# Kernel tuning notes

Hardware: AMD Instinct MI355X
Metric: run time of the kernel (lower is better)

Reference implementation:

```python
import jax, jax.numpy as jnp
import numpy as np

B, S, E, H = 4, 2048, 1024, 16
D = E // H  # head dim = 64


def setup_inputs() -> dict:
    key = jax.random.key(0)
    ks = jax.random.split(key, 5)
    scale = 0.02
    return {
        "x": jax.random.normal(ks[0], (B, S, E), dtype=jnp.float32),
        "Wa_w": jax.random.normal(ks[1], (3 * E, E), dtype=jnp.float32) * scale,
        "Wa_b": jax.random.normal(ks[2], (3 * E,), dtype=jnp.float32) * scale,
        "Wo_w": jax.random.normal(ks[3], (E, E), dtype=jnp.float32) * scale,
        "Wo_b": jax.random.normal(ks[4], (E,), dtype=jnp.float32) * scale,
    }


def reference(x, Wa_w, Wa_b, Wo_w, Wo_b):
    b, s, e = x.shape
    # Fused QKV projection (torch Linear: x @ W^T + b)
    qkv = jnp.einsum("bse,fe->bsf", x, Wa_w) + Wa_b  # [B,S,3E]
    q, k, v = jnp.split(qkv, 3, axis=-1)
    # [B,S,E] -> [B,H,S,D]
    def heads(t):
        return t.reshape(b, s, H, D).transpose(0, 2, 1, 3)
    q, k, v = heads(q), heads(k), heads(v)
    # Causal attention with explicit score matrix (as in the original)
    scores = jnp.einsum("bhqd,bhkd->bhqk", q, k) / jnp.sqrt(jnp.float32(D))
    causal = jnp.tril(jnp.ones((s, s), dtype=bool))
    scores = jnp.where(causal, scores, -jnp.inf)
    attn = jax.nn.softmax(scores, axis=-1)  # dropout p=0 -> identity
    out = jnp.einsum("bhqk,bhkd->bhqd", attn, v)  # [B,H,S,D]
    out = out.transpose(0, 2, 1, 3).reshape(b, s, e)
    return jnp.einsum("bse,fe->bsf", out, Wo_w) + Wo_b
```

## Files before the change

kernel.cpp:

```cpp
#include <hip/hip_runtime.h>
#include <hip/hip_bf16.h>
#include <cstdint>

typedef __bf16 bf16_t;
typedef __attribute__((ext_vector_type(8))) __bf16 bf16x8;
typedef __attribute__((ext_vector_type(4))) __bf16 bf16x4;
typedef __attribute__((ext_vector_type(4))) float f32x4;

#define B_ 4
#define S_ 2048
#define E_ 1024
#define H_ 16
#define D_ 64

#define QSCALE 0.18033688011112042f

__global__ void cvt_all(const float* __restrict__ x, const float* __restrict__ wa,
                        const float* __restrict__ wo,
                        bf16_t* __restrict__ xb, bf16_t* __restrict__ wab,
                        bf16_t* __restrict__ wob) {
    constexpr int N1 = (B_ * S_ * E_) / 4;
    constexpr int N2 = (3 * E_ * E_) / 4;
    constexpr int N3 = (E_ * E_) / 4;
    int i = blockIdx.x * blockDim.x + threadIdx.x;
    int stride = gridDim.x * blockDim.x;
    for (; i < N1 + N2 + N3; i += stride) {
        const float* src; bf16_t* dst; int k;
        if (i < N1) { src = x; dst = xb; k = i; }
        else if (i < N1 + N2) { src = wa; dst = wab; k = i - N1; }
        else { src = wo; dst = wob; k = i - N1 - N2; }
        f32x4 v = reinterpret_cast<const f32x4*>(src)[k];
        bf16x4 o;
        o.x = (bf16_t)v.x; o.y = (bf16_t)v.y; o.z = (bf16_t)v.z; o.w = (bf16_t)v.w;
        reinterpret_cast<bf16x4*>(dst)[k] = o;
    }
}

__device__ __forceinline__ void gload_lds16(const bf16_t* g, bf16_t* l) {
    __builtin_amdgcn_global_load_lds((const __attribute__((address_space(1))) void*)g,
                                     (__attribute__((address_space(3))) void*)l, 16, 0, 0);
}

__device__ __forceinline__ void wait_vm4() { asm volatile("s_waitcnt vmcnt(4)" ::: "memory"); }
__device__ __forceinline__ void wait_vm0() { asm volatile("s_waitcnt vmcnt(0)" ::: "memory"); }

template <int MODE>
__launch_bounds__(256, 3)
__global__ void gemm_pipe(const bf16_t* __restrict__ A, const bf16_t* __restrict__ Bm,
                          const float* __restrict__ bias,
                          int M, int N, int NG,
                          bf16_t* __restrict__ Qg, bf16_t* __restrict__ Kg,
                          bf16_t* __restrict__ Vtg, float* __restrict__ Outf) {
    constexpr int K = 1024, BK = 32, NKT = K / BK;
    constexpr int BM = 128, BN = 128;
    __shared__ __align__(16) bf16_t As[3][BM * BK];
    __shared__ __align__(16) bf16_t Bs[3][BN * BK];

    const int xcd = blockIdx.x & 7;
    const int u = blockIdx.x >> 3;
    const int grp = 8 * NG;
    const int g = u / grp, r2 = u % grp;
    const int ntl = r2 / 8, mtl = r2 & 7;
    const int mt = xcd * 8 + mtl;
    const int nt = g * NG + ntl;
    const int m0 = mt * BM, n0 = nt * BN;

    const int t = threadIdx.x;
    const int lane = t & 63;
    const int wid = t >> 6;
    const int wr = wid >> 1, wc = wid & 1;
    const int lr = lane & 15, lg = lane >> 4;

    auto mkSrc = [&](const bf16_t* base, int c, int row0) {
        const int line = c >> 3, chg = (c & 7) ^ (line & 7);
        return base + (int64_t)(row0 + 2 * line + (chg >> 2)) * K + (chg & 3) * 8;
    };
    const bf16_t* aSrc0 = mkSrc(A, t, m0);
    const bf16_t* aSrc1 = mkSrc(A, t + 256, m0);
    const bf16_t* bSrc0 = mkSrc(Bm, t, n0);
    const bf16_t* bSrc1 = mkSrc(Bm, t + 256, n0);

    auto stageT = [&](int kt, int buf) {
        gload_lds16(aSrc0 + kt * BK, &As[buf][t * 8]);
        gload_lds16(aSrc1 + kt * BK, &As[buf][(t + 256) * 8]);
        gload_lds16(bSrc0 + kt * BK, &Bs[buf][t * 8]);
        gload_lds16(bSrc1 + kt * BK, &Bs[buf][(t + 256) * 8]);
    };

    auto fragOff = [](int row, int kc) -> int {
        const int line = row >> 1;
        const int ch = ((row & 1) << 2) | kc;
        return line * 64 + ((ch ^ (line & 7)) << 3);
    };

    f32x4 acc[4][4] = {};

    stageT(0, 0);
    stageT(1, 1);

    int bufc = 0, bufs = 2;
    for (int kt = 0; kt < NKT; ++kt) {
        if (kt < NKT - 1) wait_vm4(); else wait_vm0();
        __builtin_amdgcn_s_barrier();
        __builtin_amdgcn_sched_barrier(0);

        if (kt + 2 < NKT) stageT(kt + 2, bufs);

        bf16x8 bfr[4], afr[4];
#pragma unroll
        for (int j = 0; j < 4; ++j)
            bfr[j] = *(const bf16x8*)&Bs[bufc][fragOff(wc * 64 + j * 16 + lr, lg)];
#pragma unroll
        for (int i = 0; i < 4; ++i)
            afr[i] = *(const bf16x8*)&As[bufc][fragOff(wr * 64 + i * 16 + lr, lg)];

#pragma unroll
        for (int i = 0; i < 4; ++i)
#pragma unroll
            for (int j = 0; j < 4; ++j)
                acc[i][j] = __builtin_amdgcn_mfma_f32_16x16x32_bf16(afr[i], bfr[j], acc[i][j], 0, 0, 0);

        bufc = (bufc == 2) ? 0 : bufc + 1;
        bufs = (bufs == 2) ? 0 : bufs + 1;
    }

    float bv[4];
#pragma unroll
    for (int j = 0; j < 4; ++j) bv[j] = bias[n0 + wc * 64 + j * 16 + lr];

    if (MODE == 0) {
        const int which = n0 >> 10;
        const int h = (((n0 & 1023) + wc * 64) >> 6);
#pragma unroll
        for (int i = 0; i < 4; ++i) {
#pragma unroll
            for (int r = 0; r < 4; ++r) {
                const int m = m0 + wr * 64 + i * 16 + lg * 4 + r;
                const int b = m >> 11, si = m & (S_ - 1);
                if (which == 0) {
                    bf16_t* p = &Qg[(((int64_t)(b * H_ + h)) * S_ + si) * D_ + lr];
#pragma unroll
                    for (int j = 0; j < 4; ++j)
                        p[j * 16] = (bf16_t)((acc[i][j][r] + bv[j]) * QSCALE);
                } else if (which == 1) {
                    bf16_t* p = &Kg[(((int64_t)(b * H_ + h)) * S_ + si) * D_ + lr];
#pragma unroll
                    for (int j = 0; j < 4; ++j)
                        p[j * 16] = (bf16_t)(acc[i][j][r] + bv[j]);
                } else {
                    bf16_t* p = &Vtg[(((int64_t)(b * H_ + h)) * D_ + lr) * S_ + si];
#pragma unroll
                    for (int j = 0; j < 4; ++j)
                        p[(int64_t)(j * 16) * S_] = (bf16_t)(acc[i][j][r] + bv[j]);
                }
            }
        }
    } else {
#pragma unroll
        for (int i = 0; i < 4; ++i) {
#pragma unroll
            for (int r = 0; r < 4; ++r) {
                const int m = m0 + wr * 64 + i * 16 + lg * 4 + r;
                float* p = &Outf[(int64_t)m * N + n0 + wc * 64 + lr];
#pragma unroll
                for (int j = 0; j < 4; ++j)
                    p[j * 16] = acc[i][j][r] + bv[j];
            }
        }
    }
}

__launch_bounds__(256, 4)
__global__ void attn_causal(const bf16_t* __restrict__ Qg, const bf16_t* __restrict__ Kg,
                            const bf16_t* __restrict__ Vtg, bf16_t* __restrict__ Og) {
    __shared__ __align__(16) bf16_t Ks[2][64 * 64];
    __shared__ __align__(16) bf16_t Vs[2][64 * 64];
    __shared__ __align__(16) bf16_t P_lds[4][16 * 64];

    const int bid = blockIdx.x;
    const int xcd = bid & 7, j = bid >> 3;
    const int bh = (j >> 4) * 8 + xcd;
    const int i = j & 15;
    const int qtA = i, qtB = 31 - i;

    const int t = threadIdx.x, lane = t & 63, w = t >> 6;
    const int lr = lane & 15, lg = lane >> 4;
    const int q0A = qtA * 64 + w * 16;
    const int q0B = qtB * 64 + w * 16;

    const bf16_t* Qb = Qg + (int64_t)bh * S_ * D_;
    const bf16_t* Kb = Kg + (int64_t)bh * S_ * D_;
    const bf16_t* Vb = Vtg + (int64_t)bh * D_ * S_;

    const int srow = t >> 3;
    const int scol_sw = (t & 7) ^ (srow & 7);

    auto stageK = [&](int buf, int kv0) {
        const bf16_t* base = Kb + (kv0 + srow) * D_ + scol_sw * 8;
        gload_lds16(base, &Ks[buf][t * 8]);
        gload_lds16(base + 32 * D_, &Ks[buf][t * 8 + 2048]);
    };
    auto stageV = [&](int buf, int kv0) {
        const bf16_t* base = Vb + srow * S_ + kv0 + scol_sw * 8;
        gload_lds16(base, &Vs[buf][t * 8]);
        gload_lds16(base + 32 * S_, &Vs[buf][t * 8 + 2048]);
    };

    auto psw = [](int row, int col) {
        return row * 64 + ((((col >> 3) ^ (row & 7)) << 3) | (col & 7));
    };

    bf16x8 qfA[2], qfB[2];
#pragma unroll
    for (int kk = 0; kk < 2; ++kk) {
        qfA[kk] = *(const bf16x8*)&Qb[(q0A + lr) * D_ + kk * 32 + lg * 8];
        qfB[kk] = *(const bf16x8*)&Qb[(q0B + lr) * D_ + kk * 32 + lg * 8];
    }

    bf16x8 ones;
#pragma unroll
    for (int e = 0; e < 8; ++e) ones[e] = (bf16_t)1.0f;

    f32x4 oA[4] = {}, oB[4] = {};
    f32x4 lA = {}, lB = {};

    int cur = 0;
    stageK(0, 0);
    stageV(0, 0);
    __syncthreads();

    for (int tkv = 0; tkv <= qtB; ++tkv) {
        const int kv0 = tkv * 64;
        if (tkv < qtB) { stageK(cur ^ 1, kv0 + 64); stageV(cur ^ 1, kv0 + 64); }

        auto process = [&](int q0, const bf16x8* qf, f32x4* o, f32x4& accl, bf16_t* Pw) {
            f32x4 sc[4] = {};
            __builtin_amdgcn_s_setprio(1);
#pragma unroll
            for (int nj = 0; nj < 4; ++nj) {
                if (kv0 + nj * 16 <= q0 + 15) {
                    const int krow = nj * 16 + lr;
#pragma unroll
                    for (int kk = 0; kk < 2; ++kk) {
                        bf16x8 kfr = *(const bf16x8*)&Ks[cur][krow * 64 + (((kk * 4 + lg) ^ (krow & 7)) * 8)];
                        sc[nj] = __builtin_amdgcn_mfma_f32_16x16x32_bf16(qf[kk], kfr, sc[nj], 0, 0, 0);
                    }
                }
            }
            __builtin_amdgcn_s_setprio(0);

            if (kv0 + 64 > q0) {
#pragma unroll
                for (int nj = 0; nj < 4; ++nj) {
                    const int col = kv0 + nj * 16 + lr;
#pragma unroll
                    for (int r = 0; r < 4; ++r) {
                        const int rowg = q0 + lg * 4 + r;
                        if (col > rowg) sc[nj][r] = -1e30f;
                    }
                }
            }

#pragma unroll
            for (int nj = 0; nj < 4; ++nj)
#pragma unroll
                for (int r = 0; r < 4; ++r)
                    Pw[psw(lg * 4 + r, nj * 16 + lr)] = (bf16_t)__builtin_amdgcn_exp2f(sc[nj][r]);
            asm volatile("s_waitcnt lgkmcnt(0)" ::: "memory");
            __builtin_amdgcn_sched_barrier(0);

            __builtin_amdgcn_s_setprio(1);
#pragma unroll
            for (int kk = 0; kk < 2; ++kk) {
                bf16x8 pa = *(const bf16x8*)&Pw[psw(lr, kk * 32 + lg * 8)];
                accl = __builtin_amdgcn_mfma_f32_16x16x32_bf16(pa, ones, accl, 0, 0, 0);
#pragma unroll
                for (int nd = 0; nd < 4; ++nd) {
                    const int vrow = nd * 16 + lr;
                    bf16x8 vf = *(const bf16x8*)&Vs[cur][vrow * 64 + (((kk * 4 + lg) ^ (vrow & 7)) * 8)];
                    o[nd] = __builtin_amdgcn_mfma_f32_16x16x32_bf16(pa, vf, o[nd], 0, 0, 0);
                }
            }
            __builtin_amdgcn_s_setprio(0);
        };

        process(q0B, qfB, oB, lB, &P_lds[w][0]);
        if (tkv <= qtA) process(q0A, qfA, oA, lA, &P_lds[w][0]);

        __syncthreads();
        cur ^= 1;
    }

    const int b = bh >> 4, h = bh & 15;
#pragma unroll
    for (int r = 0; r < 4; ++r) {
        const float rlA = 1.0f / lA[r];
        const float rlB = 1.0f / lB[r];
        const int rA = q0A + lg * 4 + r;
        const int rB = q0B + lg * 4 + r;
#pragma unroll
        for (int nd = 0; nd < 4; ++nd) {
            Og[((int64_t)(b * S_ + rA)) * E_ + h * D_ + nd * 16 + lr] = (bf16_t)(oA[nd][r] * rlA);
            Og[((int64_t)(b * S_ + rB)) * E_ + h * D_ + nd * 16 + lr] = (bf16_t)(oB[nd][r] * rlB);
        }
    }
}

extern "C" void kernel_launch(void* const* d_in, const int* in_sizes, int n_in,
                              void* d_out, int out_size, void* d_ws, size_t ws_size,
                              hipStream_t stream) {
    const float* x    = (const float*)d_in[0];
    const float* Wa_w = (const float*)d_in[1];
    const float* Wa_b = (const float*)d_in[2];
    const float* Wo_w = (const float*)d_in[3];
    const float* Wo_b = (const float*)d_in[4];
    float* out = (float*)d_out;

    const size_t M = (size_t)B_ * S_;
    char* ws = (char*)d_ws;
    bf16_t* xb  = (bf16_t*)ws; ws += M * E_ * 2;
    bf16_t* wab = (bf16_t*)ws; ws += (size_t)3 * E_ * E_ * 2;
    bf16_t* wob = (bf16_t*)ws; ws += (size_t)E_ * E_ * 2;
    bf16_t* Qg  = (bf16_t*)ws; ws += M * E_ * 2;
    bf16_t* Kg  = (bf16_t*)ws; ws += M * E_ * 2;
    bf16_t* Vtg = (bf16_t*)ws; ws += M * E_ * 2;
    bf16_t* Og  = (bf16_t*)ws; ws += M * E_ * 2;

    cvt_all<<<2048, 256, 0, stream>>>(x, Wa_w, Wo_w, xb, wab, wob);

    gemm_pipe<0><<<1536, 256, 0, stream>>>(
        xb, wab, Wa_b, 8192, 3072, 12, Qg, Kg, Vtg, nullptr);

    attn_causal<<<B_ * H_ * 16, 256, 0, stream>>>(Qg, Kg, Vtg, Og);

    gemm_pipe<1><<<512, 256, 0, stream>>>(
        Og, wob, Wo_b, 8192, 1024, 8, nullptr, nullptr, nullptr, out);
}
```

Baseline: 180.2 us.

## Process two M-tiles per GEMM block with continuous cross-tile prefetch

```diff
diff --git a/kernel.cpp b/kernel.cpp
--- a/kernel.cpp
+++ b/kernel.cpp
@@ -51,19 +51,19 @@
                           int M, int N, int NG,
                           bf16_t* __restrict__ Qg, bf16_t* __restrict__ Kg,
                           bf16_t* __restrict__ Vtg, float* __restrict__ Outf) {
-    constexpr int K = 1024, BK = 32, NKT = K / BK;
+    constexpr int K = 1024, BK = 32;
     constexpr int BM = 128, BN = 128;
     __shared__ __align__(16) bf16_t As[3][BM * BK];
     __shared__ __align__(16) bf16_t Bs[3][BN * BK];
 
     const int xcd = blockIdx.x & 7;
     const int u = blockIdx.x >> 3;
-    const int grp = 8 * NG;
+    const int grp = 4 * NG;
     const int g = u / grp, r2 = u % grp;
-    const int ntl = r2 / 8, mtl = r2 & 7;
-    const int mt = xcd * 8 + mtl;
+    const int ntl = r2 >> 2, q = r2 & 3;
+    const int mt0 = xcd * 8 + q;
     const int nt = g * NG + ntl;
-    const int m0 = mt * BM, n0 = nt * BN;
+    const int m0a = mt0 * BM, m0b = (mt0 + 4) * BM, n0 = nt * BN;
 
     const int t = threadIdx.x;
     const int lane = t & 63;
@@ -75,14 +75,19 @@
         const int line = c >> 3, chg = (c & 7) ^ (line & 7);
         return base + (int64_t)(row0 + 2 * line + (chg >> 2)) * K + (chg & 3) * 8;
     };
-    const bf16_t* aSrc0 = mkSrc(A, t, m0);
-    const bf16_t* aSrc1 = mkSrc(A, t + 256, m0);
+    const bf16_t* aSrcA0 = mkSrc(A, t, m0a);
+    const bf16_t* aSrcA1 = mkSrc(A, t + 256, m0a);
+    const bf16_t* aSrcB0 = mkSrc(A, t, m0b);
+    const bf16_t* aSrcB1 = mkSrc(A, t + 256, m0b);
     const bf16_t* bSrc0 = mkSrc(Bm, t, n0);
     const bf16_t* bSrc1 = mkSrc(Bm, t + 256, n0);
 
-    auto stageT = [&](int kt, int buf) {
-        gload_lds16(aSrc0 + kt * BK, &As[buf][t * 8]);
-        gload_lds16(aSrc1 + kt * BK, &As[buf][(t + 256) * 8]);
+    auto stageT = [&](int v, int buf) {
+        const int kt = v & 31;
+        const bf16_t* a0 = (v < 32) ? aSrcA0 : aSrcB0;
+        const bf16_t* a1 = (v < 32) ? aSrcA1 : aSrcB1;
+        gload_lds16(a0 + kt * BK, &As[buf][t * 8]);
+        gload_lds16(a1 + kt * BK, &As[buf][(t + 256) * 8]);
         gload_lds16(bSrc0 + kt * BK, &Bs[buf][t * 8]);
         gload_lds16(bSrc1 + kt * BK, &Bs[buf][(t + 256) * 8]);
     };
@@ -95,79 +100,98 @@
 
     f32x4 acc[4][4] = {};
 
+    float bv[4];
+#pragma unroll
+    for (int j = 0; j < 4; ++j) bv[j] = bias[n0 + wc * 64 + j * 16 + lr];
+
+    auto epi = [&](int m0) {
+        if (MODE == 0) {
+            const int which = n0 >> 10;
+            const int h = (((n0 & 1023) + wc * 64) >> 6);
+#pragma unroll
+            for (int i = 0; i < 4; ++i) {
+#pragma unroll
+                for (int r = 0; r < 4; ++r) {
+                    const int m = m0 + wr * 64 + i * 16 + lg * 4 + r;
+                    const int b = m >> 11, si = m & (S_ - 1);
+                    if (which == 0) {
+                        bf16_t* p = &Qg[(((int64_t)(b * H_ + h)) * S_ + si) * D_ + lr];
+#pragma unroll
+                        for (int j = 0; j < 4; ++j)
+                            p[j * 16] = (bf16_t)((acc[i][j][r] + bv[j]) * QSCALE);
+                    } else if (which == 1) {
+                        bf16_t* p = &Kg[(((int64_t)(b * H_ + h)) * S_ + si) * D_ + lr];
+#pragma unroll
+                        for (int j = 0; j < 4; ++j)
+                            p[j * 16] = (bf16_t)(acc[i][j][r] + bv[j]);
+                    } else {
+                        bf16_t* p = &Vtg[(((int64_t)(b * H_ + h)) * D_ + lr) * S_ + si];
+#pragma unroll
+                        for (int j = 0; j < 4; ++j)
+                            p[(int64_t)(j * 16) * S_] = (bf16_t)(acc[i][j][r] + bv[j]);
+                    }
+                }
+            }
+        } else {
+#pragma unroll
+            for (int i = 0; i < 4; ++i) {
+#pragma unroll
+                for (int r = 0; r < 4; ++r) {
+                    const int m = m0 + wr * 64 + i * 16 + lg * 4 + r;
+                    float* p = &Outf[(int64_t)m * N + n0 + wc * 64 + lr];
+#pragma unroll
+                    for (int j = 0; j < 4; ++j)
+                        p[j * 16] = acc[i][j][r] + bv[j];
+                }
+            }
+        }
+    };
+
+    auto body = [&](int v, int bufc) {
+        bf16x8 bfr[4], afr[4];
+#pragma unroll
+        for (int j = 0; j < 4; ++j)
+            bfr[j] = *(const bf16x8*)&Bs[bufc][fragOff(wc * 64 + j * 16 + lr, lg)];
+#pragma unroll
+        for (int i = 0; i < 4; ++i)
+            afr[i] = *(const bf16x8*)&As[bufc][fragOff(wr * 64 + i * 16 + lr, lg)];
+#pragma unroll
+        for (int i = 0; i < 4; ++i)
+#pragma unroll
+            for (int j = 0; j < 4; ++j)
+                acc[i][j] = __builtin_amdgcn_mfma_f32_16x16x32_bf16(afr[i], bfr[j], acc[i][j], 0, 0, 0);
+    };
+
     stageT(0, 0);
     stageT(1, 1);
 
     int bufc = 0, bufs = 2;
-    for (int kt = 0; kt < NKT; ++kt) {
-        if (kt < NKT - 1) wait_vm4(); else wait_vm0();
+    for (int v = 0; v < 32; ++v) {
+        wait_vm4();
         __builtin_amdgcn_s_barrier();
         __builtin_amdgcn_sched_barrier(0);
-
-        if (kt + 2 < NKT) stageT(kt + 2, bufs);
-
-        bf16x8 bfr[4], afr[4];
-#pragma unroll
-        for (int j = 0; j < 4; ++j)
-            bfr[j] = *(const bf16x8*)&Bs[bufc][fragOff(wc * 64 + j * 16 + lr, lg)];
-#pragma unroll
-        for (int i = 0; i < 4; ++i)
-            afr[i] = *(const bf16x8*)&As[bufc][fragOff(wr * 64 + i * 16 + lr, lg)];
-
-#pragma unroll
-        for (int i = 0; i < 4; ++i)
-#pragma unroll
-            for (int j = 0; j < 4; ++j)
-                acc[i][j] = __builtin_amdgcn_mfma_f32_16x16x32_bf16(afr[i], bfr[j], acc[i][j], 0, 0, 0);
-
+        stageT(v + 2, bufs);
+        body(v, bufc);
         bufc = (bufc == 2) ? 0 : bufc + 1;
         bufs = (bufs == 2) ? 0 : bufs + 1;
     }
-
-    float bv[4];
-#pragma unroll
-    for (int j = 0; j < 4; ++j) bv[j] = bias[n0 + wc * 64 + j * 16 + lr];
-
-    if (MODE == 0) {
-        const int which = n0 >> 10;
-        const int h = (((n0 & 1023) + wc * 64) >> 6);
-#pragma unroll
-        for (int i = 0; i < 4; ++i) {
-#pragma unroll
-            for (int r = 0; r < 4; ++r) {
-                const int m = m0 + wr * 64 + i * 16 + lg * 4 + r;
-                const int b = m >> 11, si = m & (S_ - 1);
-                if (which == 0) {
-                    bf16_t* p = &Qg[(((int64_t)(b * H_ + h)) * S_ + si) * D_ + lr];
-#pragma unroll
-                    for (int j = 0; j < 4; ++j)
-                        p[j * 16] = (bf16_t)((acc[i][j][r] + bv[j]) * QSCALE);
-                } else if (which == 1) {
-                    bf16_t* p = &Kg[(((int64_t)(b * H_ + h)) * S_ + si) * D_ + lr];
-#pragma unroll
-                    for (int j = 0; j < 4; ++j)
-                        p[j * 16] = (bf16_t)(acc[i][j][r] + bv[j]);
-                } else {
-                    bf16_t* p = &Vtg[(((int64_t)(b * H_ + h)) * D_ + lr) * S_ + si];
-#pragma unroll
-                    for (int j = 0; j < 4; ++j)
-                        p[(int64_t)(j * 16) * S_] = (bf16_t)(acc[i][j][r] + bv[j]);
-                }
-            }
-        }
-    } else {
-#pragma unroll
-        for (int i = 0; i < 4; ++i) {
-#pragma unroll
-            for (int r = 0; r < 4; ++r) {
-                const int m = m0 + wr * 64 + i * 16 + lg * 4 + r;
-                float* p = &Outf[(int64_t)m * N + n0 + wc * 64 + lr];
-#pragma unroll
-                for (int j = 0; j < 4; ++j)
-                    p[j * 16] = acc[i][j][r] + bv[j];
-            }
-        }
-    }
+    epi(m0a);
+#pragma unroll
+    for (int i = 0; i < 4; ++i)
+#pragma unroll
+        for (int j = 0; j < 4; ++j)
+            acc[i][j] = f32x4{0.f, 0.f, 0.f, 0.f};
+
+    for (int v = 32; v < 64; ++v) {
+        if (v < 63) wait_vm4(); else wait_vm0();
+        __builtin_amdgcn_s_barrier();
+        __builtin_amdgcn_sched_barrier(0);
+        if (v + 2 < 64) stageT(v + 2, bufs);
+        body(v, bufc);
+        bufc = (bufc == 2) ? 0 : bufc + 1;
+        bufs = (bufs == 2) ? 0 : bufs + 1;
+    }
+    epi(m0b);
 }
 
 __launch_bounds__(256, 4)
@@ -328,11 +352,11 @@
 
     cvt_all<<<2048, 256, 0, stream>>>(x, Wa_w, Wo_w, xb, wab, wob);
 
-    gemm_pipe<0><<<1536, 256, 0, stream>>>(
+    gemm_pipe<0><<<768, 256, 0, stream>>>(
         xb, wab, Wa_b, 8192, 3072, 12, Qg, Kg, Vtg, nullptr);
 
     attn_causal<<<B_ * H_ * 16, 256, 0, stream>>>(Qg, Kg, Vtg, Og);
 
-    gemm_pipe<1><<<512, 256, 0, stream>>>(
+    gemm_pipe<1><<<256, 256, 0, stream>>>(
         Og, wob, Wo_b, 8192, 1024, 8, nullptr, nullptr, nullptr, out);
 }
```

Measured after the change: 189.0 us. 1.05x slower.
